# Optimization experiments

Measured on AMD Instinct MI355X. Metric: run time of the kernel, lower is better.

Reference implementation:

```python
import jax, jax.numpy as jnp
import numpy as np

B, T, K = 16, 512, 128  # batch, seq_len, num_state


def setup_inputs() -> dict:
    key = jax.random.key(0)
    k1, k2, k3 = jax.random.split(key, 3)
    transition = jax.random.normal(k1, (K, K), dtype=jnp.float32)
    emission = jax.random.normal(k2, (B, T, K), dtype=jnp.float32)
    seq_lens = jax.random.randint(k3, (B,), 1, T + 1)  # lengths in [1, T]
    return {"transition": transition, "emission": emission, "seq_lens": seq_lens}


def reference(transition, emission, seq_lens):
    # potential_normalization='none' -> identity normalize().
    # combine_potentials: log phi[b, t, y_{t-1}, y_t] = trans[y_{t-1}, y_t] + emis[b, t, y_t]
    log_pot = transition[None, None, :, :] + emission[:, :, None, :]  # [B,T,K,K]

    alpha0 = emission[:, 0, :]  # [B,K]

    def step(alpha_prev, pot_t):  # alpha_prev: [B,K], pot_t: [B,K,K]
        alpha_t = jax.nn.logsumexp(alpha_prev[:, :, None] + pot_t, axis=1)
        return alpha_t, alpha_t

    # scan over time steps 1..T-1 (time-major potentials)
    _, alphas_rest = jax.lax.scan(step, alpha0, jnp.swapaxes(log_pot[:, 1:], 0, 1))
    alpha = jnp.concatenate(
        [alpha0[:, None, :], jnp.swapaxes(alphas_rest, 0, 1)], axis=1
    )  # [B,T,K]

    # gather alpha at position seq_lens - 1 per batch element
    last = jnp.take_along_axis(alpha, (seq_lens - 1)[:, None, None], axis=1)[:, 0, :]
    log_Z = jax.nn.logsumexp(last, axis=-1)  # [B]
    return alpha, log_Z
```

## Files before the change

### kernel.cpp

```cpp
#include <hip/hip_runtime.h>
#include <math.h>

#define KDIM 128
#define TLEN 512
#define BATCH 16
#define CH_L 16
#define NCH 32
#define NMAT 31

typedef _Float16 half8 __attribute__((ext_vector_type(8)));
typedef _Float16 half4 __attribute__((ext_vector_type(4)));
typedef _Float16 half2t __attribute__((ext_vector_type(2)));
typedef float floatx4 __attribute__((ext_vector_type(4)));

#if defined(__has_builtin)
#if __has_builtin(__builtin_amdgcn_fdot2)
#define HAVE_FDOT2 1
#endif
#endif

static __device__ __forceinline__ float dot2f(half2t a, half2t b, float c) {
#ifdef HAVE_FDOT2
    return __builtin_amdgcn_fdot2(a, b, c, false);
#else
    return fmaf((float)a[0], (float)b[0], fmaf((float)a[1], (float)b[1], c));
#endif
}

static __device__ __forceinline__ float dot8(const half8 v, const float4 w, float acc) {
    const uint4 r = __builtin_bit_cast(uint4, v);
    acc = dot2f(__builtin_bit_cast(half2t, w.x), __builtin_bit_cast(half2t, r.x), acc);
    acc = dot2f(__builtin_bit_cast(half2t, w.y), __builtin_bit_cast(half2t, r.y), acc);
    acc = dot2f(__builtin_bit_cast(half2t, w.z), __builtin_bit_cast(half2t, r.z), acc);
    acc = dot2f(__builtin_bit_cast(half2t, w.w), __builtin_bit_cast(half2t, r.w), acc);
    return acc;
}

static __device__ __forceinline__ void gload_lds16(const _Float16* g, _Float16* l) {
    __builtin_amdgcn_global_load_lds(
        (const __attribute__((address_space(1))) void*)g,
        (__attribute__((address_space(3))) void*)l, 16, 0, 0);
}

#define WSN_PST   0
#define WSN_SVEC  16252928
#define WSN_AENT  16506880
#define WSN_NEED  16769024

__global__ __launch_bounds__(256, 2) void crf_chunkcols2(
    const float* __restrict__ trans, const float* __restrict__ em,
    _Float16* __restrict__ Pst, float* __restrict__ Svec)
{
    const int c = blockIdx.x;
    const int b = blockIdx.y;
    const int tid = threadIdx.x;
    const int w = tid >> 6, lane = tid & 63;
    const int quad = lane >> 4, lm = lane & 15;

    __shared__ __align__(16) _Float16 Flds[128 * 136];
    __shared__ __align__(16) _Float16 Wscr[4][4608];
    __shared__ __align__(16) float gAll[16 * KDIM];

    const int t0 = c * CH_L + 1;
    const float* emb = em + (size_t)b * TLEN * KDIM;

    {
        const int m = tid & 127, kh = tid >> 7;
        #pragma unroll
        for (int kk = 0; kk < 8; ++kk) {
            const int k0 = kh * 64 + kk * 8;
            half8 o;
            #pragma unroll
            for (int j = 0; j < 8; ++j)
                o[j] = (_Float16)__expf(trans[(k0 + j) * KDIM + m]);
            *(half8*)&Flds[m * 136 + k0] = o;
        }
    }
    {
        const int i8 = tid * 8;
        const float4 e0 = *(const float4*)&emb[t0 * KDIM + i8];
        const float4 e1 = *(const float4*)&emb[t0 * KDIM + i8 + 4];
        float4 g0, g1;
        g0.x = __expf(e0.x); g0.y = __expf(e0.y); g0.z = __expf(e0.z); g0.w = __expf(e0.w);
        g1.x = __expf(e1.x); g1.y = __expf(e1.y); g1.z = __expf(e1.z); g1.w = __expf(e1.w);
        *(float4*)&gAll[i8] = g0;
        *(float4*)&gAll[i8 + 4] = g1;
    }
    __syncthreads();

    _Float16* Wb = Wscr[w];
    float sc[2];
    half8 Bf[4][2];

    #pragma unroll
    for (int nt = 0; nt < 2; ++nt) {
        float tv[4][8];
        float cm = 0.f;
        const int n = 32 * w + nt * 16 + lm;
        #pragma unroll
        for (int kt = 0; kt < 4; ++kt) {
            const int r0 = kt * 32 + quad * 8;
            const float4 ga = *(const float4*)&gAll[r0];
            const float4 gb = *(const float4*)&gAll[r0 + 4];
            const float gg[8] = {ga.x, ga.y, ga.z, ga.w, gb.x, gb.y, gb.z, gb.w};
            const float4 ta = *(const float4*)&trans[(size_t)n * KDIM + r0];
            const float4 tb = *(const float4*)&trans[(size_t)n * KDIM + r0 + 4];
            const float tt[8] = {ta.x, ta.y, ta.z, ta.w, tb.x, tb.y, tb.z, tb.w};
            #pragma unroll
            for (int j = 0; j < 8; ++j) {
                const float v = __expf(tt[j]) * gg[j];
                tv[kt][j] = v;
                cm = fmaxf(cm, v);
            }
        }
        cm = fmaxf(cm, __shfl_xor(cm, 16));
        cm = fmaxf(cm, __shfl_xor(cm, 32));
        const float ri = 1.0f / cm;
        sc[nt] = __logf(cm);
        #pragma unroll
        for (int kt = 0; kt < 4; ++kt)
            #pragma unroll
            for (int j = 0; j < 8; ++j)
                Bf[kt][nt][j] = (_Float16)(tv[kt][j] * ri);
    }

    half8 Af[8][4];
    #pragma unroll
    for (int mt = 0; mt < 8; ++mt)
        #pragma unroll
        for (int kt = 0; kt < 4; ++kt)
            Af[mt][kt] = *(const half8*)&Flds[lm * 136 + quad * 8 + mt * 2176 + kt * 32];

    const floatx4 z4 = {0.f, 0.f, 0.f, 0.f};
    for (int it = 1; it < 16; ++it) {
        #pragma unroll
        for (int nt = 0; nt < 2; ++nt) {
            floatx4 acc[8];
            #pragma unroll
            for (int mt = 0; mt < 8; ++mt)
                acc[mt] = __builtin_amdgcn_mfma_f32_16x16x32_f16(Af[mt][0], Bf[0][nt], z4, 0, 0, 0);
            #pragma unroll
            for (int kt = 1; kt < 4; ++kt)
                #pragma unroll
                for (int mt = 0; mt < 8; ++mt)
                    acc[mt] = __builtin_amdgcn_mfma_f32_16x16x32_f16(Af[mt][kt], Bf[kt][nt], acc[mt], 0, 0, 0);

            const float* g = &gAll[it * KDIM];
            float cm = 0.f;
            #pragma unroll
            for (int mt = 0; mt < 8; ++mt) {
                const float4 gv = *(const float4*)&g[mt * 16 + quad * 4];
                floatx4 v = acc[mt];
                v.x *= gv.x; v.y *= gv.y; v.z *= gv.z; v.w *= gv.w;
                acc[mt] = v;
                cm = fmaxf(cm, fmaxf(fmaxf(v.x, v.y), fmaxf(v.z, v.w)));
            }
            cm = fmaxf(cm, __shfl_xor(cm, 16));
            cm = fmaxf(cm, __shfl_xor(cm, 32));
            const float ri = 1.0f / cm;
            sc[nt] += __logf(cm);

            if (it < 15) {
                #pragma unroll
                for (int mt = 0; mt < 8; ++mt) {
                    const floatx4 v = acc[mt];
                    half4 o;
                    o[0] = (_Float16)(v.x * ri);
                    o[1] = (_Float16)(v.y * ri);
                    o[2] = (_Float16)(v.z * ri);
                    o[3] = (_Float16)(v.w * ri);
                    *(half4*)&Wb[lm * 136 + quad * 4 + nt * 2176 + mt * 16] = o;
                }
            } else {
                #pragma unroll
                for (int mt = 0; mt < 8; ++mt) {
                    const floatx4 v = acc[mt];
                    const int ba = quad * 144 + lm + mt * 576 + nt * 16;
                    Wb[ba]       = (_Float16)(v.x * ri);
                    Wb[ba + 36]  = (_Float16)(v.y * ri);
                    Wb[ba + 72]  = (_Float16)(v.z * ri);
                    Wb[ba + 108] = (_Float16)(v.w * ri);
                }
            }
        }
        asm volatile("s_waitcnt lgkmcnt(0)" ::: "memory");
        if (it < 15) {
            #pragma unroll
            for (int kt = 0; kt < 4; ++kt)
                #pragma unroll
                for (int nt = 0; nt < 2; ++nt)
                    Bf[kt][nt] = *(const half8*)&Wb[lm * 136 + quad * 8 + nt * 2176 + kt * 32];
        }
    }

    _Float16* Pc = Pst + ((size_t)(b * NMAT + c)) * 16384;
    #pragma unroll
    for (int Kl = 0; Kl < 4; ++Kl)
        #pragma unroll
        for (int h = 0; h < 2; ++h) {
            const half4 lo = *(const half4*)&Wb[(2 * lane + h) * 36 + Kl * 8];
            const half4 hi = *(const half4*)&Wb[(2 * lane + h) * 36 + Kl * 8 + 4];
            half8 v;
            #pragma unroll
            for (int e = 0; e < 4; ++e) { v[e] = lo[e]; v[4 + e] = hi[e]; }
            const int u = (2 * (4 * w + Kl) + h) * 64 + lane;
            *(half8*)&Pc[(size_t)u * 8] = v;
        }
    if (quad == 0) {
        float* sp = Svec + ((size_t)(b * NMAT + c)) * KDIM + 32 * w;
        sp[lm] = sc[0];
        sp[lm + 16] = sc[1];
    }
}

__global__ __launch_bounds__(64, 1) void crf_scanw4(
    const float* __restrict__ em, const _Float16* __restrict__ Pst,
    const float* __restrict__ Svec, float* __restrict__ aEnter)
{
    const int b = blockIdx.x;
    const int lane = threadIdx.x;
    const int j0 = 2 * lane;

    __shared__ __align__(16) _Float16 Pbuf[3][16384];
    __shared__ __align__(16) _Float16 pbuf[KDIM];

    const _Float16* Pb = Pst + (size_t)b * NMAT * 16384;
    const float* svb = Svec + (size_t)b * NMAT * KDIM;
    float* aeb = aEnter + (size_t)b * NCH * KDIM;

    #pragma unroll
    for (int i = 0; i < 32; ++i)
        gload_lds16(Pb + i * 512 + lane * 8, &Pbuf[0][i * 512]);
    #pragma unroll
    for (int i = 0; i < 32; ++i)
        gload_lds16(Pb + 16384 + i * 512 + lane * 8, &Pbuf[1][i * 512]);

    float2 a0 = *(const float2*)&em[(size_t)b * TLEN * KDIM + j0];
    float mx = fmaxf(a0.x, a0.y);
    #pragma unroll
    for (int o = 32; o; o >>= 1) mx = fmaxf(mx, __shfl_xor(mx, o));
    *(float2*)&aeb[j0] = a0;
    float lq0 = a0.x - mx, lq1 = a0.y - mx;
    float L = mx;
    float2 sv = *(const float2*)&svb[j0];

    int cb = 0;
    for (int c = 0; c < NMAT; ++c) {
        if (c + 1 < NMAT) {
            asm volatile("s_waitcnt vmcnt(32)" ::: "memory");
        } else {
            asm volatile("s_waitcnt vmcnt(0)" ::: "memory");
        }

        if (c + 2 < NMAT) {
            const _Float16* src = Pb + (size_t)(c + 2) * 16384;
            _Float16* dst = &Pbuf[(cb + 2) % 3][0];
            #pragma unroll
            for (int i = 0; i < 32; ++i)
                gload_lds16(src + i * 512 + lane * 8, &dst[i * 512]);
        }

        const float v0 = lq0 + sv.x, v1 = lq1 + sv.y;
        float M = fmaxf(v0, v1);
        #pragma unroll
        for (int o = 32; o; o >>= 1) M = fmaxf(M, __shfl_xor(M, o));
        half2t p2;
        p2[0] = (_Float16)__expf(v0 - M);
        p2[1] = (_Float16)__expf(v1 - M);
        ((half2t*)pbuf)[lane] = p2;
        if (c + 1 < NMAT) sv = *(const float2*)&svb[(size_t)(c + 1) * KDIM + j0];

        const _Float16* Pcur = &Pbuf[cb][0];
        float q0 = 0.f, q1 = 0.f;
        #pragma unroll
        for (int K = 0; K < 16; ++K) {
            const float4 wv = *(const float4*)&pbuf[K * 8];
            const half8 c0 = *(const half8*)&Pcur[((2 * K + 0) * 64 + lane) * 8];
            const half8 c1 = *(const half8*)&Pcur[((2 * K + 1) * 64 + lane) * 8];
            q0 = dot8(c0, wv, q0);
            q1 = dot8(c1, wv, q1);
        }

        const float base = L + M;
        const float lg0 = __logf(q0), lg1 = __logf(q1);
        float2 st;
        st.x = base + lg0;
        st.y = base + lg1;
        *(float2*)&aeb[(size_t)(c + 1) * KDIM + j0] = st;
        lq0 = lg0;
        lq1 = lg1;
        L = base;
        cb = (cb + 1) % 3;
    }
}

__global__ __launch_bounds__(64, 1) void crf_replayw(
    const float* __restrict__ trans, const float* __restrict__ em,
    const int* __restrict__ seq_lens, const float* __restrict__ aEnter,
    float* __restrict__ alpha, float* __restrict__ logZ)
{
    const int c = blockIdx.x, b = blockIdx.y;
    const int l = threadIdx.x;

    __shared__ __align__(16) _Float16 pbuf[KDIM];

    half2t Ea[64], Eb[64];
    #pragma unroll
    for (int t2 = 0; t2 < 64; ++t2) {
        const float* r0 = &trans[(2 * t2) * KDIM];
        const float* r1 = &trans[(2 * t2 + 1) * KDIM];
        half2t ea, eb;
        ea[0] = (_Float16)__expf(r0[l]);
        ea[1] = (_Float16)__expf(r1[l]);
        eb[0] = (_Float16)__expf(r0[l + 64]);
        eb[1] = (_Float16)__expf(r1[l + 64]);
        Ea[t2] = ea;
        Eb[t2] = eb;
    }

    const int len = seq_lens[b];
    const float* emb = em + (size_t)b * TLEN * KDIM;
    float* outb = alpha + (size_t)b * TLEN * KDIM;
    const float* ae = aEnter + ((size_t)b * NCH + c) * KDIM;

    float a0 = ae[l], a1 = ae[l + 64];
    if (c == 0) {
        a0 = emb[l];
        a1 = emb[l + 64];
    }
    float mx = fmaxf(a0, a1);
    #pragma unroll
    for (int o = 32; o; o >>= 1) mx = fmaxf(mx, __shfl_xor(mx, o));
    float L = mx;
    pbuf[l]      = (_Float16)__expf(a0 - L);
    pbuf[l + 64] = (_Float16)__expf(a1 - L);

    float la0 = 0.f, la1 = -INFINITY;
    if (c == 0) {
        outb[l] = a0;
        outb[l + 64] = a1;
        if (len == 1) { la0 = a0; la1 = a1; }
    }

    const int t_begin = c * CH_L + 1;
    const int t_end = (c == NCH - 1) ? (TLEN - 1) : (c * CH_L + CH_L);

    float e0 = emb[t_begin * KDIM + l];
    float e1 = emb[t_begin * KDIM + l + 64];

    for (int t = t_begin; t <= t_end; ++t) {
        float n0 = 0.f, n1 = 0.f;
        if (t < t_end) {
            n0 = emb[(t + 1) * KDIM + l];
            n1 = emb[(t + 1) * KDIM + l + 64];
        }

        float q0 = 0.f, q1 = 0.f;
        #pragma unroll
        for (int s = 0; s < 16; ++s) {
            const float4 w = *(const float4*)&pbuf[s * 8];
            const half2t p0 = __builtin_bit_cast(half2t, w.x);
            const half2t p1 = __builtin_bit_cast(half2t, w.y);
            const half2t p2 = __builtin_bit_cast(half2t, w.z);
            const half2t p3 = __builtin_bit_cast(half2t, w.w);
            q0 = dot2f(p0, Ea[4 * s + 0], q0);
            q0 = dot2f(p1, Ea[4 * s + 1], q0);
            q0 = dot2f(p2, Ea[4 * s + 2], q0);
            q0 = dot2f(p3, Ea[4 * s + 3], q0);
            q1 = dot2f(p0, Eb[4 * s + 0], q1);
            q1 = dot2f(p1, Eb[4 * s + 1], q1);
            q1 = dot2f(p2, Eb[4 * s + 2], q1);
            q1 = dot2f(p3, Eb[4 * s + 3], q1);
        }

        const float A0 = e0 + L + __logf(q0);
        const float A1 = e1 + L + __logf(q1);
        outb[t * KDIM + l] = A0;
        outb[t * KDIM + l + 64] = A1;
        if (t == len - 1) { la0 = A0; la1 = A1; }

        const float sigma = __shfl(q0, 0);
        const float ri = 1.0f / sigma;
        pbuf[l]      = (_Float16)(q0 * ri * __expf(e0));
        pbuf[l + 64] = (_Float16)(q1 * ri * __expf(e1));
        L += __logf(sigma);
        e0 = n0; e1 = n1;
    }

    const bool blockowns = (len == 1) ? (c == 0) : (((len - 2) >> 4) == c);
    if (blockowns) {
        float m2 = fmaxf(la0, la1);
        #pragma unroll
        for (int o = 32; o; o >>= 1) m2 = fmaxf(m2, __shfl_xor(m2, o));
        float e = __expf(la0 - m2) + __expf(la1 - m2);
        #pragma unroll
        for (int o = 32; o; o >>= 1) e += __shfl_xor(e, o);
        if (l == 0) logZ[b] = m2 + __logf(e);
    }
}

__global__ __launch_bounds__(256) void crf_forward_fallback(
    const float* __restrict__ trans, const float* __restrict__ em,
    const int* __restrict__ seq_lens, float* __restrict__ alpha_out,
    float* __restrict__ logZ_out)
{
    const int b = blockIdx.x;
    const int tid = threadIdx.x;
    const int j = tid & (KDIM - 1);
    const int h = tid >> 7;

    __shared__ __align__(16) float p_lds[KDIM];
    __shared__ float part[KDIM];
    __shared__ float red[8];

    float Ereg[64];
    #pragma unroll
    for (int k = 0; k < 64; ++k) Ereg[k] = __expf(trans[(h * 64 + k) * KDIM + j]);

    const int len = seq_lens[b];
    const float* emb = em + (size_t)b * TLEN * KDIM;
    float* outb = alpha_out + (size_t)b * TLEN * KDIM;

    float a = 0.f, last_a = 0.f;
    if (h == 0) {
        a = emb[j];
        outb[j] = a;
        if (len == 1) last_a = a;
    }
    for (int t = 1; t < TLEN; ++t) {
        {
            float v = (h == 0) ? a : -INFINITY;
            #pragma unroll
            for (int o = 32; o >= 1; o >>= 1) v = fmaxf(v, __shfl_xor(v, o));
            if ((tid & 63) == 0) red[tid >> 6] = v;
        }
        __syncthreads();
        const float m = fmaxf(red[0], red[1]);
        if (h == 0) p_lds[j] = __expf(a - m);
        __syncthreads();
        float em_t = 0.f;
        if (h == 0) em_t = emb[t * KDIM + j];
        float acc0 = 0.f, acc1 = 0.f, acc2 = 0.f, acc3 = 0.f;
        const float4* p4 = (const float4*)(p_lds + h * 64);
        #pragma unroll
        for (int k4 = 0; k4 < 16; ++k4) {
            float4 pv = p4[k4];
            acc0 = fmaf(pv.x, Ereg[4 * k4 + 0], acc0);
            acc1 = fmaf(pv.y, Ereg[4 * k4 + 1], acc1);
            acc2 = fmaf(pv.z, Ereg[4 * k4 + 2], acc2);
            acc3 = fmaf(pv.w, Ereg[4 * k4 + 3], acc3);
        }
        const float acc = (acc0 + acc1) + (acc2 + acc3);
        if (h == 1) part[j] = acc;
        __syncthreads();
        if (h == 0) {
            const float q = acc + part[j];
            a = em_t + m + __logf(q);
            outb[t * KDIM + j] = a;
            if (t == len - 1) last_a = a;
        }
    }
    {
        float v = (h == 0) ? last_a : -INFINITY;
        #pragma unroll
        for (int o = 32; o >= 1; o >>= 1) v = fmaxf(v, __shfl_xor(v, o));
        if ((tid & 63) == 0) red[tid >> 6] = v;
    }
    __syncthreads();
    const float m2 = fmaxf(red[0], red[1]);
    float e = (h == 0) ? __expf(last_a - m2) : 0.f;
    #pragma unroll
    for (int o = 32; o >= 1; o >>= 1) e += __shfl_xor(e, o);
    if ((tid & 63) == 0) red[4 + (tid >> 6)] = e;
    __syncthreads();
    if (tid == 0) logZ_out[b] = m2 + logf(red[4] + red[5]);
}

extern "C" void kernel_launch(void* const* d_in, const int* in_sizes, int n_in,
                              void* d_out, int out_size, void* d_ws, size_t ws_size,
                              hipStream_t stream) {
    const float* trans    = (const float*)d_in[0];
    const float* em       = (const float*)d_in[1];
    const int*   seq_lens = (const int*)d_in[2];

    float* alpha_out = (float*)d_out;
    float* logZ_out  = alpha_out + (size_t)BATCH * TLEN * KDIM;

    char* ws = (char*)d_ws;

    if (ws_size >= (size_t)WSN_NEED) {
        _Float16* Pst  = (_Float16*)(ws + WSN_PST);
        float*    Svec = (float*)(ws + WSN_SVEC);
        float*    aEnt = (float*)(ws + WSN_AENT);
        crf_chunkcols2<<<dim3(NMAT, BATCH), 256, 0, stream>>>(trans, em, Pst, Svec);
        crf_scanw4<<<BATCH, 64, 0, stream>>>(em, Pst, Svec, aEnt);
        crf_replayw<<<dim3(NCH, BATCH), 64, 0, stream>>>(trans, em, seq_lens, aEnt,
                                                         alpha_out, logZ_out);
    } else {
        crf_forward_fallback<<<BATCH, 256, 0, stream>>>(trans, em, seq_lens,
                                                        alpha_out, logZ_out);
    }
}
```

Before: 156.4 us.

## Use two waves per chunk block with 64 columns each, staging B in LDS

The chunk-product kernel now runs 128 threads (two waves) per block instead of four, and each wave handles 64 output columns (four 16-wide tiles) rather than 32. The B operand is no longer kept in registers across iterations. It is written to a per-wave LDS scratch with a 144-element row stride and reloaded for each tile, which removes the explicit waitcnt and the separate last-iteration transposed store path. The final export to Pst now gathers columns directly from LDS. This halves the block's waves and likely lowers occupancy, while adding LDS traffic per tile. In exchange each wave reuses its register-resident A fragments over twice as many columns.

```diff
diff --git a/kernel.cpp b/kernel.cpp
--- a/kernel.cpp
+++ b/kernel.cpp
@@ -47,7 +47,7 @@
 #define WSN_AENT  16506880
 #define WSN_NEED  16769024
 
-__global__ __launch_bounds__(256, 2) void crf_chunkcols2(
+__global__ __launch_bounds__(128, 1) void crf_chunkcols3(
     const float* __restrict__ trans, const float* __restrict__ em,
     _Float16* __restrict__ Pst, float* __restrict__ Svec)
 {
@@ -58,17 +58,17 @@
     const int quad = lane >> 4, lm = lane & 15;
 
     __shared__ __align__(16) _Float16 Flds[128 * 136];
-    __shared__ __align__(16) _Float16 Wscr[4][4608];
+    __shared__ __align__(16) _Float16 Wscr[2][9216];
     __shared__ __align__(16) float gAll[16 * KDIM];
 
     const int t0 = c * CH_L + 1;
     const float* emb = em + (size_t)b * TLEN * KDIM;
 
     {
-        const int m = tid & 127, kh = tid >> 7;
-        #pragma unroll
-        for (int kk = 0; kk < 8; ++kk) {
-            const int k0 = kh * 64 + kk * 8;
+        const int m = tid;
+        #pragma unroll
+        for (int kk = 0; kk < 16; ++kk) {
+            const int k0 = kk * 8;
             half8 o;
             #pragma unroll
             for (int j = 0; j < 8; ++j)
@@ -76,27 +76,24 @@
             *(half8*)&Flds[m * 136 + k0] = o;
         }
     }
-    {
-        const int i8 = tid * 8;
-        const float4 e0 = *(const float4*)&emb[t0 * KDIM + i8];
-        const float4 e1 = *(const float4*)&emb[t0 * KDIM + i8 + 4];
-        float4 g0, g1;
-        g0.x = __expf(e0.x); g0.y = __expf(e0.y); g0.z = __expf(e0.z); g0.w = __expf(e0.w);
-        g1.x = __expf(e1.x); g1.y = __expf(e1.y); g1.z = __expf(e1.z); g1.w = __expf(e1.w);
-        *(float4*)&gAll[i8] = g0;
-        *(float4*)&gAll[i8 + 4] = g1;
+    #pragma unroll
+    for (int s = 0; s < 4; ++s) {
+        const int i4 = (tid + s * 128) * 4;
+        const float4 e = *(const float4*)&emb[t0 * KDIM + i4];
+        float4 gv;
+        gv.x = __expf(e.x); gv.y = __expf(e.y); gv.z = __expf(e.z); gv.w = __expf(e.w);
+        *(float4*)&gAll[i4] = gv;
     }
     __syncthreads();
 
     _Float16* Wb = Wscr[w];
-    float sc[2];
-    half8 Bf[4][2];
-
-    #pragma unroll
-    for (int nt = 0; nt < 2; ++nt) {
+    float sc[4];
+
+    #pragma unroll
+    for (int nt = 0; nt < 4; ++nt) {
         float tv[4][8];
         float cm = 0.f;
-        const int n = 32 * w + nt * 16 + lm;
+        const int n = 64 * w + nt * 16 + lm;
         #pragma unroll
         for (int kt = 0; kt < 4; ++kt) {
             const int r0 = kt * 32 + quad * 8;
@@ -118,10 +115,12 @@
         const float ri = 1.0f / cm;
         sc[nt] = __logf(cm);
         #pragma unroll
-        for (int kt = 0; kt < 4; ++kt)
-            #pragma unroll
-            for (int j = 0; j < 8; ++j)
-                Bf[kt][nt][j] = (_Float16)(tv[kt][j] * ri);
+        for (int kt = 0; kt < 4; ++kt) {
+            half8 o;
+            #pragma unroll
+            for (int j = 0; j < 8; ++j) o[j] = (_Float16)(tv[kt][j] * ri);
+            *(half8*)&Wb[(nt * 16 + lm) * 144 + kt * 32 + quad * 8] = o;
+        }
     }
 
     half8 Af[8][4];
@@ -134,16 +133,21 @@
     const floatx4 z4 = {0.f, 0.f, 0.f, 0.f};
     for (int it = 1; it < 16; ++it) {
         #pragma unroll
-        for (int nt = 0; nt < 2; ++nt) {
+        for (int nt = 0; nt < 4; ++nt) {
+            half8 Bf[4];
+            #pragma unroll
+            for (int kt = 0; kt < 4; ++kt)
+                Bf[kt] = *(const half8*)&Wb[(nt * 16 + lm) * 144 + kt * 32 + quad * 8];
+
             floatx4 acc[8];
             #pragma unroll
             for (int mt = 0; mt < 8; ++mt)
-                acc[mt] = __builtin_amdgcn_mfma_f32_16x16x32_f16(Af[mt][0], Bf[0][nt], z4, 0, 0, 0);
+                acc[mt] = __builtin_amdgcn_mfma_f32_16x16x32_f16(Af[mt][0], Bf[0], z4, 0, 0, 0);
             #pragma unroll
             for (int kt = 1; kt < 4; ++kt)
                 #pragma unroll
                 for (int mt = 0; mt < 8; ++mt)
-                    acc[mt] = __builtin_amdgcn_mfma_f32_16x16x32_f16(Af[mt][kt], Bf[kt][nt], acc[mt], 0, 0, 0);
+                    acc[mt] = __builtin_amdgcn_mfma_f32_16x16x32_f16(Af[mt][kt], Bf[kt], acc[mt], 0, 0, 0);
 
             const float* g = &gAll[it * KDIM];
             float cm = 0.f;
@@ -160,56 +164,35 @@
             const float ri = 1.0f / cm;
             sc[nt] += __logf(cm);
 
-            if (it < 15) {
-                #pragma unroll
-                for (int mt = 0; mt < 8; ++mt) {
-                    const floatx4 v = acc[mt];
-                    half4 o;
-                    o[0] = (_Float16)(v.x * ri);
-                    o[1] = (_Float16)(v.y * ri);
-                    o[2] = (_Float16)(v.z * ri);
-                    o[3] = (_Float16)(v.w * ri);
-                    *(half4*)&Wb[lm * 136 + quad * 4 + nt * 2176 + mt * 16] = o;
-                }
-            } else {
-                #pragma unroll
-                for (int mt = 0; mt < 8; ++mt) {
-                    const floatx4 v = acc[mt];
-                    const int ba = quad * 144 + lm + mt * 576 + nt * 16;
-                    Wb[ba]       = (_Float16)(v.x * ri);
-                    Wb[ba + 36]  = (_Float16)(v.y * ri);
-                    Wb[ba + 72]  = (_Float16)(v.z * ri);
-                    Wb[ba + 108] = (_Float16)(v.w * ri);
-                }
+            #pragma unroll
+            for (int mt = 0; mt < 8; ++mt) {
+                const floatx4 v = acc[mt];
+                half4 o;
+                o[0] = (_Float16)(v.x * ri);
+                o[1] = (_Float16)(v.y * ri);
+                o[2] = (_Float16)(v.z * ri);
+                o[3] = (_Float16)(v.w * ri);
+                *(half4*)&Wb[(nt * 16 + lm) * 144 + mt * 16 + quad * 4] = o;
             }
         }
-        asm volatile("s_waitcnt lgkmcnt(0)" ::: "memory");
-        if (it < 15) {
-            #pragma unroll
-            for (int kt = 0; kt < 4; ++kt)
-                #pragma unroll
-                for (int nt = 0; nt < 2; ++nt)
-                    Bf[kt][nt] = *(const half8*)&Wb[lm * 136 + quad * 8 + nt * 2176 + kt * 32];
-        }
     }
 
     _Float16* Pc = Pst + ((size_t)(b * NMAT + c)) * 16384;
     #pragma unroll
-    for (int Kl = 0; Kl < 4; ++Kl)
+    for (int Kl = 0; Kl < 8; ++Kl)
         #pragma unroll
         for (int h = 0; h < 2; ++h) {
-            const half4 lo = *(const half4*)&Wb[(2 * lane + h) * 36 + Kl * 8];
-            const half4 hi = *(const half4*)&Wb[(2 * lane + h) * 36 + Kl * 8 + 4];
             half8 v;
             #pragma unroll
-            for (int e = 0; e < 4; ++e) { v[e] = lo[e]; v[4 + e] = hi[e]; }
-            const int u = (2 * (4 * w + Kl) + h) * 64 + lane;
+            for (int e = 0; e < 8; ++e)
+                v[e] = Wb[(Kl * 8 + e) * 144 + 2 * lane + h];
+            const int u = (2 * (8 * w + Kl) + h) * 64 + lane;
             *(half8*)&Pc[(size_t)u * 8] = v;
         }
     if (quad == 0) {
-        float* sp = Svec + ((size_t)(b * NMAT + c)) * KDIM + 32 * w;
-        sp[lm] = sc[0];
-        sp[lm + 16] = sc[1];
+        float* sp = Svec + ((size_t)(b * NMAT + c)) * KDIM + 64 * w;
+        #pragma unroll
+        for (int nt = 0; nt < 4; ++nt) sp[nt * 16 + lm] = sc[nt];
     }
 }
 
@@ -492,7 +475,7 @@
         _Float16* Pst  = (_Float16*)(ws + WSN_PST);
         float*    Svec = (float*)(ws + WSN_SVEC);
         float*    aEnt = (float*)(ws + WSN_AENT);
-        crf_chunkcols2<<<dim3(NMAT, BATCH), 256, 0, stream>>>(trans, em, Pst, Svec);
+        crf_chunkcols3<<<dim3(NMAT, BATCH), 128, 0, stream>>>(trans, em, Pst, Svec);
         crf_scanw4<<<BATCH, 64, 0, stream>>>(em, Pst, Svec, aEnt);
         crf_replayw<<<dim3(NCH, BATCH), 64, 0, stream>>>(trans, em, seq_lens, aEnt,
                                                          alpha_out, logZ_out);
```

After: 189.0 us. +20.8%, slower.

## Split chunk scan across four waves with register-resident double-buffered matrices

Applied to the files above, without the earlier changes.

The serial chunk-boundary scan kernel now runs 256 threads per batch instead of one wave. Each wave holds a quarter of the fp16 transfer matrix in registers, double-buffered from global memory, replacing the triple-buffered LDS prefetch. Partial dot products are reduced through shared memory each step, which adds two extra barriers per chunk. An s_waitcnt in the chunk-matrix kernel is also dropped, which could affect correctness of LDS reads there.

```diff
diff --git a/kernel.cpp b/kernel.cpp
--- a/kernel.cpp
+++ b/kernel.cpp
@@ -36,16 +36,11 @@
     return acc;
 }
 
-static __device__ __forceinline__ void gload_lds16(const _Float16* g, _Float16* l) {
-    __builtin_amdgcn_global_load_lds(
-        (const __attribute__((address_space(1))) void*)g,
-        (__attribute__((address_space(3))) void*)l, 16, 0, 0);
-}
-
 #define WSN_PST   0
 #define WSN_SVEC  16252928
 #define WSN_AENT  16506880
 #define WSN_NEED  16769024
+
 
 __global__ __launch_bounds__(256, 2) void crf_chunkcols2(
     const float* __restrict__ trans, const float* __restrict__ em,
@@ -183,7 +178,6 @@
                 }
             }
         }
-        asm volatile("s_waitcnt lgkmcnt(0)" ::: "memory");
         if (it < 15) {
             #pragma unroll
             for (int kt = 0; kt < 4; ++kt)
@@ -197,13 +191,13 @@
     #pragma unroll
     for (int Kl = 0; Kl < 4; ++Kl)
         #pragma unroll
-        for (int h = 0; h < 2; ++h) {
-            const half4 lo = *(const half4*)&Wb[(2 * lane + h) * 36 + Kl * 8];
-            const half4 hi = *(const half4*)&Wb[(2 * lane + h) * 36 + Kl * 8 + 4];
+        for (int hh = 0; hh < 2; ++hh) {
+            const half4 lo = *(const half4*)&Wb[(2 * lane + hh) * 36 + Kl * 8];
+            const half4 hi = *(const half4*)&Wb[(2 * lane + hh) * 36 + Kl * 8 + 4];
             half8 v;
             #pragma unroll
             for (int e = 0; e < 4; ++e) { v[e] = lo[e]; v[4 + e] = hi[e]; }
-            const int u = (2 * (4 * w + Kl) + h) * 64 + lane;
+            const int u = (2 * (4 * w + Kl) + hh) * 64 + lane;
             *(half8*)&Pc[(size_t)u * 8] = v;
         }
     if (quad == 0) {
@@ -213,84 +207,93 @@
     }
 }
 
-__global__ __launch_bounds__(64, 1) void crf_scanw4(
+__global__ __launch_bounds__(256, 1) void crf_scanw6(
     const float* __restrict__ em, const _Float16* __restrict__ Pst,
     const float* __restrict__ Svec, float* __restrict__ aEnter)
 {
     const int b = blockIdx.x;
-    const int lane = threadIdx.x;
-    const int j0 = 2 * lane;
-
-    __shared__ __align__(16) _Float16 Pbuf[3][16384];
+    const int tid = threadIdx.x;
+    const int w = tid >> 6, lane = tid & 63;
+
     __shared__ __align__(16) _Float16 pbuf[KDIM];
+    __shared__ __align__(16) float part[4][KDIM];
+    __shared__ float red[2];
 
     const _Float16* Pb = Pst + (size_t)b * NMAT * 16384;
     const float* svb = Svec + (size_t)b * NMAT * KDIM;
     float* aeb = aEnter + (size_t)b * NCH * KDIM;
 
-    #pragma unroll
-    for (int i = 0; i < 32; ++i)
-        gload_lds16(Pb + i * 512 + lane * 8, &Pbuf[0][i * 512]);
-    #pragma unroll
-    for (int i = 0; i < 32; ++i)
-        gload_lds16(Pb + 16384 + i * 512 + lane * 8, &Pbuf[1][i * 512]);
-
-    float2 a0 = *(const float2*)&em[(size_t)b * TLEN * KDIM + j0];
-    float mx = fmaxf(a0.x, a0.y);
-    #pragma unroll
-    for (int o = 32; o; o >>= 1) mx = fmaxf(mx, __shfl_xor(mx, o));
-    *(float2*)&aeb[j0] = a0;
-    float lq0 = a0.x - mx, lq1 = a0.y - mx;
-    float L = mx;
-    float2 sv = *(const float2*)&svb[j0];
-
-    int cb = 0;
-    for (int c = 0; c < NMAT; ++c) {
-        if (c + 1 < NMAT) {
-            asm volatile("s_waitcnt vmcnt(32)" ::: "memory");
-        } else {
-            asm volatile("s_waitcnt vmcnt(0)" ::: "memory");
-        }
-
+    half8 PA[8], PB[8];
+    #pragma unroll
+    for (int i = 0; i < 8; ++i)
+        PA[i] = *(const half8*)&Pb[((8 * w + i) * 64 + lane) * 8];
+    #pragma unroll
+    for (int i = 0; i < 8; ++i)
+        PB[i] = *(const half8*)&Pb[16384 + ((8 * w + i) * 64 + lane) * 8];
+
+    float lq = 0.f, L = 0.f, svR = 0.f, svN = 0.f;
+    {
+        float a0 = -INFINITY;
+        if (tid < KDIM) a0 = em[(size_t)b * TLEN * KDIM + tid];
+        float m = a0;
+        #pragma unroll
+        for (int o = 32; o; o >>= 1) m = fmaxf(m, __shfl_xor(m, o));
+        if (w < 2 && lane == 0) red[w] = m;
+        __syncthreads();
+        const float mx = fmaxf(red[0], red[1]);
+        if (tid < KDIM) {
+            aeb[tid] = a0;
+            lq = a0 - mx;
+            L = mx;
+            svR = svb[tid];
+        }
+        __syncthreads();
+    }
+
+    auto STEP = [&](half8 (&P)[8], int c) {
+        if (w < 2) {
+            float m = lq + svR;
+            #pragma unroll
+            for (int o = 32; o; o >>= 1) m = fmaxf(m, __shfl_xor(m, o));
+            if (lane == 0) red[w] = m;
+        }
+        __syncthreads();
+        const float M = fmaxf(red[0], red[1]);
+        if (w < 2) {
+            pbuf[tid] = (_Float16)__expf(lq + svR - M);
+            if (c + 1 < NMAT) svN = svb[(size_t)(c + 1) * KDIM + tid];
+        }
+        __syncthreads();
+        float q0 = 0.f, q1 = 0.f;
+        #pragma unroll
+        for (int kk = 0; kk < 4; ++kk) {
+            const float4 wv = *(const float4*)&pbuf[(4 * w + kk) * 8];
+            q0 = dot8(P[2 * kk + 0], wv, q0);
+            q1 = dot8(P[2 * kk + 1], wv, q1);
+        }
+        float2 qq; qq.x = q0; qq.y = q1;
+        *(float2*)&part[w][2 * lane] = qq;
         if (c + 2 < NMAT) {
-            const _Float16* src = Pb + (size_t)(c + 2) * 16384;
-            _Float16* dst = &Pbuf[(cb + 2) % 3][0];
-            #pragma unroll
-            for (int i = 0; i < 32; ++i)
-                gload_lds16(src + i * 512 + lane * 8, &dst[i * 512]);
-        }
-
-        const float v0 = lq0 + sv.x, v1 = lq1 + sv.y;
-        float M = fmaxf(v0, v1);
-        #pragma unroll
-        for (int o = 32; o; o >>= 1) M = fmaxf(M, __shfl_xor(M, o));
-        half2t p2;
-        p2[0] = (_Float16)__expf(v0 - M);
-        p2[1] = (_Float16)__expf(v1 - M);
-        ((half2t*)pbuf)[lane] = p2;
-        if (c + 1 < NMAT) sv = *(const float2*)&svb[(size_t)(c + 1) * KDIM + j0];
-
-        const _Float16* Pcur = &Pbuf[cb][0];
-        float q0 = 0.f, q1 = 0.f;
-        #pragma unroll
-        for (int K = 0; K < 16; ++K) {
-            const float4 wv = *(const float4*)&pbuf[K * 8];
-            const half8 c0 = *(const half8*)&Pcur[((2 * K + 0) * 64 + lane) * 8];
-            const half8 c1 = *(const half8*)&Pcur[((2 * K + 1) * 64 + lane) * 8];
-            q0 = dot8(c0, wv, q0);
-            q1 = dot8(c1, wv, q1);
-        }
-
-        const float base = L + M;
-        const float lg0 = __logf(q0), lg1 = __logf(q1);
-        float2 st;
-        st.x = base + lg0;
-        st.y = base + lg1;
-        *(float2*)&aeb[(size_t)(c + 1) * KDIM + j0] = st;
-        lq0 = lg0;
-        lq1 = lg1;
-        L = base;
-        cb = (cb + 1) % 3;
+            #pragma unroll
+            for (int i = 0; i < 8; ++i)
+                P[i] = *(const half8*)&Pb[(size_t)(c + 2) * 16384
+                                          + ((8 * w + i) * 64 + lane) * 8];
+        }
+        __syncthreads();
+        if (tid < KDIM) {
+            const float q = part[0][tid] + part[1][tid]
+                          + part[2][tid] + part[3][tid];
+            const float lg = __logf(q);
+            aeb[(size_t)(c + 1) * KDIM + tid] = L + M + lg;
+            lq = lg;
+            L += M;
+            svR = svN;
+        }
+    };
+
+    for (int c = 0; c < NMAT; c += 2) {
+        STEP(PA, c);
+        if (c + 1 < NMAT) STEP(PB, c + 1);
     }
 }
 
@@ -493,7 +496,7 @@
         float*    Svec = (float*)(ws + WSN_SVEC);
         float*    aEnt = (float*)(ws + WSN_AENT);
         crf_chunkcols2<<<dim3(NMAT, BATCH), 256, 0, stream>>>(trans, em, Pst, Svec);
-        crf_scanw4<<<BATCH, 64, 0, stream>>>(em, Pst, Svec, aEnt);
+        crf_scanw6<<<BATCH, 256, 0, stream>>>(em, Pst, Svec, aEnt);
         crf_replayw<<<dim3(NCH, BATCH), 64, 0, stream>>>(trans, em, seq_lens, aEnt,
                                                          alpha_out, logZ_out);
     } else {
```

Result: faster. 152.7 us (-2.4%).
